# Optimization experiments

Hardware: AMD Instinct MI355X
Metric: run time of the kernel (lower is better)

The kernel has to match this reference:

```python
import jax, jax.numpy as jnp
import numpy as np
from jax import lax

B, Q, H, W = 2, 2304, 64, 64
ENC_OUT = 64          # encoder out_dim
DIM = 192             # base_dim
HEAD = 8
R = 3
RA = (2 * R + 1) ** 2  # 49 local-window positions
CF = 64                # pe enc_dims // 2 (complex channels)
ENC_DIMS = 2 * CF      # 128
IN_DIM = (DIM + ENC_DIMS) * RA + 2  # 15682
HID = 256


def conv3(x, w, b):
    y = lax.conv_general_dilated(x, w, (1, 1), 'SAME',
                                 dimension_numbers=('NCHW', 'OIHW', 'NCHW'))
    return y + b[None, :, None, None]


def _flat_gather(img, idx):
    # img [B,C,HW], idx [B,...] -> [B,C,...]
    return jax.vmap(lambda f, i: f[:, i])(img, idx)


def gather_nearest(img, c):
    # grid_sample nearest, align_corners=False, zeros padding. c [B,Q,K,2] (y,x)
    Bc, C, Hc, Wc = img.shape
    py = ((c[..., 0] + 1) * Hc - 1) / 2
    px = ((c[..., 1] + 1) * Wc - 1) / 2
    iy = jnp.round(py); ix = jnp.round(px)
    valid = (iy >= 0) & (iy < Hc) & (ix >= 0) & (ix < Wc)
    idx = (jnp.clip(iy, 0, Hc - 1) * Wc + jnp.clip(ix, 0, Wc - 1)).astype(jnp.int32)
    g = _flat_gather(img.reshape(Bc, C, Hc * Wc), idx)  # [B,C,Q,K]
    g = jnp.where(valid[:, None], g, 0.0)
    return g.transpose(0, 2, 3, 1)  # [B,Q,K,C]


def gather_bilinear_zeros(img, c):
    # grid_sample bilinear, align_corners=False, zeros padding. c [B,Q,K,2]
    Bc, C, Hc, Wc = img.shape
    py = ((c[..., 0] + 1) * Hc - 1) / 2
    px = ((c[..., 1] + 1) * Wc - 1) / 2
    y0f = jnp.floor(py); x0f = jnp.floor(px)
    wy = py - y0f; wx = px - x0f
    y0 = y0f.astype(jnp.int32); x0 = x0f.astype(jnp.int32)
    flat = img.reshape(Bc, C, Hc * Wc)
    def corner(yi, xi, w):
        valid = (yi >= 0) & (yi < Hc) & (xi >= 0) & (xi < Wc)
        idx = jnp.clip(yi, 0, Hc - 1) * Wc + jnp.clip(xi, 0, Wc - 1)
        return _flat_gather(flat, idx) * (w * valid)[:, None]
    out = (corner(y0, x0, (1 - wy) * (1 - wx)) + corner(y0, x0 + 1, (1 - wy) * wx)
           + corner(y0 + 1, x0, wy * (1 - wx)) + corner(y0 + 1, x0 + 1, wy * wx))
    return out.transpose(0, 2, 3, 1)


def gather_bilinear_border(img, c):
    # grid_sample bilinear, align_corners=False, border padding. c [B,Q,2]
    Bc, C, Hc, Wc = img.shape
    py = jnp.clip(((c[..., 0] + 1) * Hc - 1) / 2, 0, Hc - 1)
    px = jnp.clip(((c[..., 1] + 1) * Wc - 1) / 2, 0, Wc - 1)
    y0f = jnp.floor(py); x0f = jnp.floor(px)
    wy = py - y0f; wx = px - x0f
    y0 = y0f.astype(jnp.int32); x0 = x0f.astype(jnp.int32)
    y1 = jnp.minimum(y0 + 1, Hc - 1); x1 = jnp.minimum(x0 + 1, Wc - 1)
    flat = img.reshape(Bc, C, Hc * Wc)
    g = lambda yi, xi: _flat_gather(flat, yi * Wc + xi)  # [B,C,Q]
    out = (g(y0, x0) * ((1 - wy) * (1 - wx))[:, None]
           + g(y0, x1) * ((1 - wy) * wx)[:, None]
           + g(y1, x0) * (wy * (1 - wx))[:, None]
           + g(y1, x1) * (wy * wx)[:, None])
    return out.transpose(0, 2, 1)  # [B,Q,C]


def _forward(inp, coord, cell, enc_w, enc_b, qw, qb, kw, kb, vw, vb, fw, fb,
             pbw, pbb, pew, w1, b1, w2, b2):
    feat = conv3(inp, enc_w, enc_b)            # encoder (simplified)
    fq = conv3(feat, qw, qb); fk = conv3(feat, kw, kb)
    fv = conv3(feat, vw, vb); ff = conv3(feat, fw, fb)
    Bq, Qn = coord.shape[:2]
    Hf, Wf = feat.shape[-2:]
    dk = DIM // HEAD
    c = jnp.clip(coord, -1 + 1e-6, 1 - 1e-6)[:, :, None, :]   # [B,Q,1,2]
    # nearest feature-grid pixel-center coordinates (= grid_sample nearest of coord_lr)
    iy = jnp.round(((c[..., 0] + 1) * Hf - 1) / 2)
    ix = jnp.round(((c[..., 1] + 1) * Wf - 1) / 2)
    ck0 = jnp.stack([-1 + (2 * iy + 1) / Hf, -1 + (2 * ix + 1) / Wf], axis=-1)
    dh = jnp.linspace(-R, R, 2 * R + 1) * 2 / Hf
    dw = jnp.linspace(-R, R, 2 * R + 1) * 2 / Wf
    delta = jnp.stack(jnp.meshgrid(dh, dw, indexing='ij'), axis=-1).reshape(1, 1, RA, 2)
    ck = ck0 + delta                                          # [B,Q,49,2]
    q_ = gather_bilinear_zeros(fq, c)[:, :, 0].reshape(Bq, Qn, HEAD, dk)
    k_ = gather_nearest(fk, ck).reshape(Bq, Qn, RA, HEAD, dk)
    v_ = gather_nearest(fv, ck).reshape(Bq, Qn, RA, HEAD, dk)
    fr = gather_nearest(ff, ck)                               # [B,Q,49,CF]
    hw = jnp.array([Hf, Wf], dtype=coord.dtype)
    rel = (coord[:, :, None, :] - ck) * hw                    # [B,Q,49,2]
    rel_cell = cell * hw
    sim = jnp.einsum('bqhd,bqkhd->bqkh', q_, k_) / np.sqrt(dk).astype(np.float32)
    pb = rel @ pbw + pbb                                      # positional bias [B,Q,49,HEAD]
    attn = jax.nn.softmax(sim + pb, axis=2)                   # softmax over the 49 window slots
    attn_map = attn[0, 10, :, 0].reshape(2 * R + 1, 2 * R + 1, 1)
    v_weighted = (v_ * attn[..., None]).reshape(Bq, Qn, RA, DIM)
    frc = jnp.fft.fft2(fr.reshape(Bq, Qn, 2 * R + 1, 2 * R + 1, CF),
                       axes=(2, 3), norm='ortho').reshape(Bq, Qn, RA, CF)
    phase = rel @ pew                                         # Fourier PE: exp(i*phase)
    enc = lax.complex(jnp.cos(phase), jnp.sin(phase)) * frc
    enc = jnp.stack([enc.real, enc.imag], axis=-1).reshape(Bq, Qn, RA, ENC_DIMS)
    out = jnp.concatenate([v_weighted, enc], axis=-1).reshape(Bq, Qn, -1)
    out = jnp.concatenate([out, rel_cell], axis=-1)           # [B,Q,IN_DIM]
    pred = jax.nn.relu(out @ w1 + b1) @ w2 + b2               # imnet MLP
    ret = pred + gather_bilinear_border(inp, coord)           # global residual
    return ret, attn_map


def setup_inputs() -> dict:
    key = jax.random.key(0)
    ks = jax.random.split(key, 20)
    def n(k, shape, s=0.05):
        return jax.random.normal(k, shape, dtype=jnp.float32) * s
    inp = jax.random.normal(ks[0], (B, 3, H, W), dtype=jnp.float32)
    coord = jax.random.uniform(ks[1], (B, Q, 2), minval=-1.0, maxval=1.0, dtype=jnp.float32)
    cell = jnp.full((B, Q, 2), 2.0 / 128, dtype=jnp.float32)
    return {
        'inp': inp, 'coord': coord, 'cell': cell,
        'enc_w': n(ks[2], (ENC_OUT, 3, 3, 3)), 'enc_b': n(ks[3], (ENC_OUT,)),
        'qw': n(ks[4], (DIM, ENC_OUT, 3, 3)), 'qb': n(ks[5], (DIM,)),
        'kw': n(ks[6], (DIM, ENC_OUT, 3, 3)), 'kb': n(ks[7], (DIM,)),
        'vw': n(ks[8], (DIM, ENC_OUT, 3, 3)), 'vb': n(ks[9], (DIM,)),
        'fw': n(ks[10], (CF, ENC_OUT, 3, 3)), 'fb': n(ks[11], (CF,)),
        'pbw': n(ks[12], (2, HEAD), 0.5), 'pbb': n(ks[13], (HEAD,), 0.5),
        'pew': n(ks[14], (2, CF), 0.5),
        'w1': n(ks[15], (IN_DIM, HID), 0.01), 'b1': n(ks[16], (HID,)),
        'w2': n(ks[17], (HID, 3), 0.05), 'b2': n(ks[18], (3,)),
    }


def reference(inp, coord, cell, enc_w, enc_b, qw, qb, kw, kb, vw, vb, fw, fb,
              pbw, pbb, pew, w1, b1, w2, b2):
    return _forward(inp, coord, cell, enc_w, enc_b, qw, qb, kw, kb, vw, vb,
                    fw, fb, pbw, pbb, pew, w1, b1, w2, b2)
```

## Files before the change

kernel.cpp:

```cpp
#include <hip/hip_runtime.h>

typedef unsigned short u16t;
typedef unsigned int   u32t;
typedef __attribute__((ext_vector_type(8))) short short8;
typedef __attribute__((ext_vector_type(4))) float f32x4;

#define B_    2
#define QN    2304
#define NQ    4608
#define HWS   64
#define ENCC  64
#define DIMC  192
#define NHEAD 8
#define DKH   24
#define RAW   49
#define CFC   64
#define FRP   68
#define CMAP  640
#define KCONV 576
#define INDIM 15682
#define KPAD  15744
#define HIDN  256
#define PIX   8192
#define SPLITK 12
#define KSLICE (KPAD/SPLITK)

__device__ __forceinline__ float b2f(u16t u){ u32t v=((u32t)u)<<16; return __builtin_bit_cast(float,v); }
__device__ __forceinline__ u16t f2b(float f){ u32t v=__builtin_bit_cast(u32t,f); return (u16t)((v + 0x7FFFu + ((v>>16)&1u))>>16); }

#define GLOAD16(SRC, DST) __builtin_amdgcn_global_load_lds( \
  (const __attribute__((address_space(1))) unsigned int*)(const void*)(SRC), \
  (__attribute__((address_space(3))) unsigned int*)(void*)(DST), 16, 0, 0)

__global__ __launch_bounds__(256) void k_enc(const float* __restrict__ inp, const float* __restrict__ ew,
                      const float* __restrict__ eb, u16t* __restrict__ feat){
  int i = blockIdx.x*256+threadIdx.x;
  if(i>=B_*HWS*HWS*ENCC) return;
  int oc=i&63, x=(i>>6)&63, y=(i>>12)&63, b=i>>18;
  float acc = eb[oc];
  for(int c=0;c<3;c++)
    for(int dy=0;dy<3;dy++){
      int yy=y+dy-1; if(yy<0||yy>=HWS) continue;
      for(int dx=0;dx<3;dx++){
        int xx=x+dx-1; if(xx<0||xx>=HWS) continue;
        acc += inp[((b*3+c)*HWS+yy)*HWS+xx] * ew[((oc*3+c)*3+dy)*3+dx];
      }
    }
  feat[i]=f2b(acc);
}

__global__ __launch_bounds__(256) void k_w1t(const float* __restrict__ w1, u16t* __restrict__ w1t){
  __shared__ u16t t[64][65];
  int kb = blockIdx.x*64, nb = blockIdx.y*64;
  for(int i=threadIdx.x;i<4096;i+=256){
    int k=i>>6, n=i&63; int gk=kb+k;
    t[k][n] = (gk<INDIM) ? f2b(w1[(size_t)gk*HIDN + nb + n]) : (u16t)0;
  }
  __syncthreads();
  for(int i=threadIdx.x;i<4096;i+=256){
    int n=i>>6, k=i&63;
    w1t[(size_t)(nb+n)*KPAD + kb + k] = t[k][n];
  }
}

__global__ __launch_bounds__(256) void k_wconv(const float* qw,const float* kw,const float* vw,const float* fw,
                        const float* qb,const float* kb_,const float* vb,const float* fb,
                        u16t* __restrict__ wct, float* __restrict__ bias){
  int i = blockIdx.x*256+threadIdx.x;
  if(i < CMAP*KCONV){
    int oc=i/KCONV, kk=i%KCONV;
    int ic=kk&63, tap=kk>>6;
    const float* w; int ol=oc;
    if(oc<192) w=qw;
    else if(oc<384){w=kw; ol=oc-192;}
    else if(oc<576){w=vw; ol=oc-384;}
    else {w=fw; ol=oc-576;}
    wct[(size_t)oc*KCONV + kk] = f2b(w[(ol*64+ic)*9 + tap]);
  }
  if(i<CMAP){
    bias[i] = (i<192)? qb[i] : (i<384? kb_[i-192] : (i<576? vb[i-384] : fb[i-576]));
  }
}

__global__ __launch_bounds__(256) void k_im2col(const u16t* __restrict__ feat, u16t* __restrict__ A){
  int i = blockIdx.x*256+threadIdx.x;
  if(i>=PIX*72) return;
  int k8=i%72, pix=i/72;
  int tap=k8/8, ic8=(k8&7)<<3;
  int x=pix&63, y=(pix>>6)&63, b=pix>>12;
  int yy=y+tap/3-1, xx=x+tap%3-1;
  uint4 v;
  if(yy>=0&&yy<HWS&&xx>=0&&xx<HWS) v = *(const uint4*)&feat[(size_t)(((b*HWS+yy)*HWS+xx)*ENCC)+ic8];
  else v = make_uint4(0u,0u,0u,0u);
  *(uint4*)&A[(size_t)pix*KCONV + tap*64 + ic8] = v;
}

__global__ __launch_bounds__(256,2) void k_gemm128(const u16t* __restrict__ A, int lda,
    const u16t* __restrict__ BT, int ldb, const float* __restrict__ bias,
    void* __restrict__ Cout, int ldc, int kslice, int mode){
  __shared__ __align__(16) u16t As[128*32];
  __shared__ __align__(16) u16t Bs[128*32];
  int m0 = blockIdx.x*128, n0 = blockIdx.y*128;
  int tid = threadIdx.x;
  int wave = tid>>6, lane = tid&63;
  int wm = wave>>1, wn = wave&1;
  int kg = lane>>4, l16 = lane&15;
  int kbeg = blockIdx.z*kslice, kend = kbeg+kslice;
  f32x4 acc[4][4] = {};
  for(int k0=kbeg;k0<kend;k0+=32){
    __syncthreads();
    #pragma unroll
    for(int s=0;s<2;s++){
      int seg = (wave*2+s)*64 + lane;
      int row = seg>>2, qp = seg&3;
      int q = qp ^ ((row>>1)&3);
      GLOAD16(&A [(size_t)(m0+row)*lda + k0 + q*8], &As[(wave*2+s)*512]);
      GLOAD16(&BT[(size_t)(n0+row)*ldb + k0 + q*8], &Bs[(wave*2+s)*512]);
    }
    __syncthreads();
    short8 a[4], b[4];
    #pragma unroll
    for(int mf=0;mf<4;mf++){
      int row = wm*64+mf*16+l16;
      a[mf] = *(const short8*)&As[row*32 + (kg^((row>>1)&3))*8];
    }
    #pragma unroll
    for(int nf=0;nf<4;nf++){
      int row = wn*64+nf*16+l16;
      b[nf] = *(const short8*)&Bs[row*32 + (kg^((row>>1)&3))*8];
    }
    #pragma unroll
    for(int mf=0;mf<4;mf++)
      #pragma unroll
      for(int nf=0;nf<4;nf++)
        acc[mf][nf] = __builtin_amdgcn_mfma_f32_16x16x32_bf16(a[mf], b[nf], acc[mf][nf], 0,0,0);
  }
  int l4 = lane>>4;
  if(mode==0){
    u16t* C16 = (u16t*)Cout;
    #pragma unroll
    for(int mf=0;mf<4;mf++){
      #pragma unroll
      for(int nf=0;nf<4;nf++){
        #pragma unroll
        for(int r=0;r<4;r++){
          int gm = m0 + wm*64 + mf*16 + l4*4 + r;
          int gn = n0 + wn*64 + nf*16 + l16;
          C16[(size_t)gm*ldc+gn] = f2b(acc[mf][nf][r] + bias[gn]);
        }
      }
    }
  } else {
    float* C32 = (float*)Cout + (size_t)blockIdx.z * (size_t)(gridDim.x*128) * ldc;
    #pragma unroll
    for(int mf=0;mf<4;mf++){
      #pragma unroll
      for(int nf=0;nf<4;nf++){
        #pragma unroll
        for(int r=0;r<4;r++){
          int gm = m0 + wm*64 + mf*16 + l4*4 + r;
          int gn = n0 + wn*64 + nf*16 + l16;
          C32[(size_t)gm*ldc+gn] = acc[mf][nf][r];
        }
      }
    }
  }
}

__global__ __launch_bounds__(256) void k_redout(const float* __restrict__ hidp, const float* __restrict__ b1,
                      const float* __restrict__ w2, const float* __restrict__ b2v,
                      const float* __restrict__ inp, const float* __restrict__ coord,
                      float* __restrict__ outp, int M, int q0){
  int i = blockIdx.x*256+threadIdx.x;
  if(i>=M*64) return;
  int q=i>>6, lane=i&63, n4=lane*4;
  f32x4 acc = *(const f32x4*)&b1[n4];
  for(int s=0;s<SPLITK;s++)
    acc += *(const f32x4*)&hidp[((size_t)s*M + q)*HIDN + n4];
  float h0=fmaxf(acc.x,0.f), h1=fmaxf(acc.y,0.f), h2=fmaxf(acc.z,0.f), h3=fmaxf(acc.w,0.f);
  float p0 = h0*w2[n4*3+0] + h1*w2[(n4+1)*3+0] + h2*w2[(n4+2)*3+0] + h3*w2[(n4+3)*3+0];
  float p1 = h0*w2[n4*3+1] + h1*w2[(n4+1)*3+1] + h2*w2[(n4+2)*3+1] + h3*w2[(n4+3)*3+1];
  float p2 = h0*w2[n4*3+2] + h1*w2[(n4+1)*3+2] + h2*w2[(n4+2)*3+2] + h3*w2[(n4+3)*3+2];
  #pragma unroll
  for(int m=1;m<64;m<<=1){
    p0 += __shfl_xor(p0, m);
    p1 += __shfl_xor(p1, m);
    p2 += __shfl_xor(p2, m);
  }
  if(lane<3){
    int qg = q0 + q;
    int j = lane;
    float accj = (j==0? p0 : (j==1? p1 : p2)) + b2v[j];
    int b=qg/QN;
    float cy=coord[qg*2], cx=coord[qg*2+1];
    float py=fminf(fmaxf(((cy+1.f)*64.f-1.f)*0.5f,0.f),63.f);
    float px=fminf(fmaxf(((cx+1.f)*64.f-1.f)*0.5f,0.f),63.f);
    float y0f=floorf(py), x0f=floorf(px);
    float wy=py-y0f, wx=px-x0f;
    int y0=(int)y0f, x0=(int)x0f;
    int y1=min(y0+1,63), x1=min(x0+1,63);
    const float* ip=&inp[(size_t)(b*3+j)*4096];
    float g00=ip[y0*64+x0], g01=ip[y0*64+x1];
    float g10=ip[y1*64+x0], g11=ip[y1*64+x1];
    float res=g00*(1.f-wy)*(1.f-wx)+g01*(1.f-wy)*wx+g10*wy*(1.f-wx)+g11*wy*wx;
    outp[qg*3+j]=accj+res;
  }
}

__global__ __launch_bounds__(256) void k_feat(const float* __restrict__ coord, const float* __restrict__ cell,
                       const u16t* __restrict__ maps, const float* __restrict__ pbw,
                       const float* __restrict__ pbb, const float* __restrict__ pew,
                       u16t* __restrict__ F, float* __restrict__ outAttn, int q0){
  __shared__ float q_lds[DIMC];
  __shared__ float relsy[RAW], relsx[RAW];
  __shared__ int   wbase[RAW];
  __shared__ float sa[RAW][NHEAD];
  __shared__ float fr_lds[RAW*FRP];
  __shared__ float c7[7], s7[7];
  __shared__ float pewf0[CFC], pewf1[CFC];
  __shared__ float pbwf0[NHEAD], pbwf1[NHEAD], pbbf[NHEAD];

  int qg = q0 + blockIdx.x;
  int b  = qg / QN;
  int tid = threadIdx.x;
  float cy = coord[qg*2], cx = coord[qg*2+1];
  const float lo = -1.0f + 1e-6f, hi = 1.0f - 1e-6f;
  float ccy = fminf(fmaxf(cy,lo),hi), ccx = fminf(fmaxf(cx,lo),hi);
  float pyq = ((ccy+1.f)*64.f - 1.f)*0.5f, pxq = ((ccx+1.f)*64.f - 1.f)*0.5f;
  int iy = (int)rintf(pyq), ix = (int)rintf(pxq);

  if(tid < RAW){
    int ki = tid/7, kj = tid%7;
    int yy = iy + ki - 3, xx = ix + kj - 3;
    wbase[tid] = (yy>=0&&yy<64&&xx>=0&&xx<64) ? ((b*64+yy)*64+xx)*CMAP : -1;
    float ck_y = (-1.f + (float)(2*iy+1)*(1.f/64.f)) + (float)(ki-3)*(2.f/64.f);
    float ck_x = (-1.f + (float)(2*ix+1)*(1.f/64.f)) + (float)(kj-3)*(2.f/64.f);
    relsy[tid] = (cy - ck_y)*64.f;
    relsx[tid] = (cx - ck_x)*64.f;
  }
  if(tid<7){ float ang = -6.283185307179586f * (float)tid / 7.f; c7[tid]=cosf(ang); s7[tid]=sinf(ang); }
  if(tid<CFC){ pewf0[tid]=pew[tid]; pewf1[tid]=pew[CFC+tid]; }
  if(tid<NHEAD){ pbwf0[tid]=pbw[tid]; pbwf1[tid]=pbw[NHEAD+tid]; pbbf[tid]=pbb[tid]; }
  __syncthreads();

  if(tid < DIMC){
    float y0f=floorf(pyq), x0f=floorf(pxq);
    float wy=pyq-y0f, wx=pxq-x0f;
    int y0=(int)y0f, x0=(int)x0f;
    float acc=0.f;
    for(int ty=0;ty<2;ty++) for(int tx=0;tx<2;tx++){
      int yy=y0+ty, xx=x0+tx;
      if(yy<0||yy>=64||xx<0||xx>=64) continue;
      float w=(ty? wy:1.f-wy)*(tx? wx:1.f-wx);
      acc += w * b2f(maps[(size_t)((b*64+yy)*64+xx)*CMAP + tid]);
    }
    q_lds[tid]=acc;
  }
  for(int i=tid;i<RAW*8;i+=256){
    int k=i>>3, c8=(i&7)<<3;
    int base=wbase[k];
    f32x4 lo4={0.f,0.f,0.f,0.f}, hi4={0.f,0.f,0.f,0.f};
    if(base>=0){
      uint4 t = *(const uint4*)&maps[(size_t)base + 576 + c8];
      lo4 = f32x4{b2f((u16t)t.x), b2f((u16t)(t.x>>16)), b2f((u16t)t.y), b2f((u16t)(t.y>>16))};
      hi4 = f32x4{b2f((u16t)t.z), b2f((u16t)(t.z>>16)), b2f((u16t)t.w), b2f((u16t)(t.w>>16))};
    }
    *(f32x4*)&fr_lds[k*FRP+c8]   = lo4;
    *(f32x4*)&fr_lds[k*FRP+c8+4] = hi4;
  }
  __syncthreads();

  for(int i=tid;i<RAW*NHEAD;i+=256){
    int k=i>>3, h=i&7;
    int base=wbase[k];
    float dot=0.f;
    if(base>=0){
      const u16t* p = &maps[(size_t)base + DIMC + h*DKH];
      for(int c8=0;c8<3;c8++){
        uint4 t = *(const uint4*)&p[c8*8];
        u32t a4[4]={t.x,t.y,t.z,t.w};
        for(int j=0;j<4;j++){
          dot += q_lds[h*DKH + c8*8 + 2*j]   * b2f((u16t)a4[j]);
          dot += q_lds[h*DKH + c8*8 + 2*j+1] * b2f((u16t)(a4[j]>>16));
        }
      }
    }
    sa[k][h] = dot/sqrtf(24.f) + relsy[k]*pbwf0[h] + relsx[k]*pbwf1[h] + pbbf[h];
  }
  __syncthreads();

  if(tid < 64){
    int h = tid>>3, sub = tid&7;
    float m = -1e30f;
    for(int k=sub;k<RAW;k+=8) m = fmaxf(m, sa[k][h]);
    #pragma unroll
    for(int mm=1;mm<8;mm<<=1) m = fmaxf(m, __shfl_xor(m, mm));
    float s = 0.f;
    for(int k=sub;k<RAW;k+=8){ float e=__expf(sa[k][h]-m); sa[k][h]=e; s+=e; }
    #pragma unroll
    for(int mm=1;mm<8;mm<<=1) s += __shfl_xor(s, mm);
    float inv = 1.f/s;
    for(int k=sub;k<RAW;k+=8) sa[k][h]*=inv;
  }
  __syncthreads();
  if(qg==10 && tid<RAW) outAttn[tid] = sa[tid][0];

  size_t frow = (size_t)(qg-q0)*KPAD;
  for(int i=tid;i<RAW*24;i+=256){
    int k=i/24, c8=(i%24)*8;
    int base=wbase[k];
    u32t o[4]={0,0,0,0};
    if(base>=0){
      uint4 t = *(const uint4*)&maps[(size_t)base + 384 + c8];
      u32t a4[4]={t.x,t.y,t.z,t.w};
      for(int j=0;j<4;j++){
        int c0=c8+2*j;
        u16t r0=f2b(b2f((u16t)a4[j])      * sa[k][ c0   /DKH]);
        u16t r1=f2b(b2f((u16t)(a4[j]>>16))* sa[k][(c0+1)/DKH]);
        o[j] = (u32t)r0 | ((u32t)r1<<16);
      }
    }
    *(uint4*)&F[frow + (size_t)k*320 + c8] = make_uint4(o[0],o[1],o[2],o[3]);
  }
  if(tid<64){
    int idx=INDIM-2+tid;
    u16t v=0;
    if(idx==15680) v=f2b(cell[qg*2]*64.f);
    else if(idx==15681) v=f2b(cell[qg*2+1]*64.f);
    F[frow+idx]=v;
  }

  #pragma unroll
  for(int pp=0;pp<2;pp++){
    int p = tid + pp*256;
    if(p < 448){
      int v_ = p>>6, c = p&63;
      float Gr[7], Gi[7];
      #pragma unroll
      for(int a_=0;a_<7;a_++){
        float re=0.f, im=0.f;
        #pragma unroll
        for(int bb=0;bb<7;bb++){
          float f=fr_lds[(a_*7+bb)*FRP+c];
          int m=(v_*bb)%7;
          re += f*c7[m]; im += f*s7[m];
        }
        Gr[a_]=re; Gi[a_]=im;
      }
      float pw0=pewf0[c], pw1=pewf1[c];
      #pragma unroll
      for(int u=0;u<7;u++){
        int k = u*7 + v_;
        float tr=0.f, ti=0.f;
        #pragma unroll
        for(int a_=0;a_<7;a_++){
          int m=(u*a_)%7;
          float cc=c7[m], ss=s7[m];
          tr += Gr[a_]*cc - Gi[a_]*ss;
          ti += Gr[a_]*ss + Gi[a_]*cc;
        }
        tr*=(1.f/7.f); ti*=(1.f/7.f);
        float ph = relsy[k]*pw0 + relsx[k]*pw1;
        float sp, cp; __sincosf(ph, &sp, &cp);
        float er = cp*tr - sp*ti, ei = cp*ti + sp*tr;
        u32t pk = (u32t)f2b(er) | ((u32t)f2b(ei)<<16);
        *(u32t*)&F[frow + (size_t)k*320 + 192 + 2*c] = pk;
      }
    }
  }
}

__global__ __launch_bounds__(256) void k_mark(float* __restrict__ outp, int n, float val){
  int i = blockIdx.x*256+threadIdx.x;
  if(i<n) outp[i]=val;
}

extern "C" void kernel_launch(void* const* d_in, const int* in_sizes, int n_in,
                              void* d_out, int out_size, void* d_ws, size_t ws_size,
                              hipStream_t stream){
  int I_inp, I_coord, I_cell, I_encw, I_encb, I_qw, I_qb, I_kw, I_kb, I_vw, I_vb,
      I_fw, I_fb, I_pbw, I_pbb, I_pew, I_w1, I_b1, I_w2, I_b2;
  bool dictOrder = (n_in==20 && in_sizes[0]==24576 && in_sizes[1]==9216 && in_sizes[3]==1728
                    && in_sizes[5]==110592 && in_sizes[16]==4014592 && in_sizes[19]==3);
  bool sortOrder = (n_in==20 && in_sizes[0]==256 && in_sizes[1]==3 && in_sizes[8]==24576
                    && in_sizes[10]==110592 && in_sizes[18]==4014592 && in_sizes[19]==768);
  if(dictOrder){
    I_inp=0; I_coord=1; I_cell=2; I_encw=3; I_encb=4; I_qw=5; I_qb=6; I_kw=7; I_kb=8;
    I_vw=9; I_vb=10; I_fw=11; I_fb=12; I_pbw=13; I_pbb=14; I_pew=15; I_w1=16; I_b1=17; I_w2=18; I_b2=19;
  } else if(sortOrder){
    I_b1=0; I_b2=1; I_cell=2; I_coord=3; I_encb=4; I_encw=5; I_fb=6; I_fw=7; I_inp=8;
    I_kb=9; I_kw=10; I_pbb=11; I_pbw=12; I_pew=13; I_qb=14; I_qw=15; I_vb=16; I_vw=17; I_w1=18; I_w2=19;
  } else {
    float mark = (float)(n_in==20 ? in_sizes[0] : 1000000+n_in);
    k_mark<<<dim3((out_size+255)/256), dim3(256), 0, stream>>>((float*)d_out, out_size, mark);
    return;
  }

  const float* inp  =(const float*)d_in[I_inp];
  const float* coord=(const float*)d_in[I_coord];
  const float* cell =(const float*)d_in[I_cell];
  const float* enc_w=(const float*)d_in[I_encw];
  const float* enc_b=(const float*)d_in[I_encb];
  const float* qw=(const float*)d_in[I_qw];
  const float* qb=(const float*)d_in[I_qb];
  const float* kw=(const float*)d_in[I_kw];
  const float* kbp=(const float*)d_in[I_kb];
  const float* vw=(const float*)d_in[I_vw];
  const float* vb=(const float*)d_in[I_vb];
  const float* fw=(const float*)d_in[I_fw];
  const float* fb=(const float*)d_in[I_fb];
  const float* pbw=(const float*)d_in[I_pbw];
  const float* pbb=(const float*)d_in[I_pbb];
  const float* pew=(const float*)d_in[I_pew];
  const float* w1=(const float*)d_in[I_w1];
  const float* b1=(const float*)d_in[I_b1];
  const float* w2=(const float*)d_in[I_w2];
  const float* b2v=(const float*)d_in[I_b2];
  float* outp=(float*)d_out;

  char* ws=(char*)d_ws;
  size_t off=0;
  auto alloc=[&](size_t bytes){ size_t o=off; off=(off+bytes+255)&~(size_t)255; return o; };
  size_t o_feat = alloc((size_t)PIX*ENCC*2);
  size_t o_imc  = alloc((size_t)PIX*KCONV*2);
  size_t o_wct  = alloc((size_t)CMAP*KCONV*2);
  size_t o_cb   = alloc((size_t)CMAP*4);
  size_t o_maps = alloc((size_t)PIX*CMAP*2);
  size_t o_w1t  = alloc((size_t)HIDN*KPAD*2);
  size_t fixed = off;
  size_t rem = (ws_size>fixed)? ws_size-fixed : 0;
  size_t perQ = (size_t)KPAD*2 + (size_t)SPLITK*HIDN*4;
  long long cq = (long long)(rem/perQ);
  int chunkQ = (int)((cq/128)*128);
  if(chunkQ>NQ) chunkQ=NQ;
  size_t o_F, o_hp;
  if(chunkQ>=128){
    o_F  = alloc((size_t)chunkQ*KPAD*2);
    o_hp = alloc((size_t)SPLITK*chunkQ*HIDN*4);
  } else {
    chunkQ = 128;
    o_F  = o_imc;
    o_hp = (o_imc + (size_t)128*KPAD*2 + 255) & ~(size_t)255;
  }

  u16t*  feat=(u16t*)(ws+o_feat);
  u16t*  imc =(u16t*)(ws+o_imc);
  u16t*  wct =(u16t*)(ws+o_wct);
  float* cbias=(float*)(ws+o_cb);
  u16t*  maps=(u16t*)(ws+o_maps);
  u16t*  w1t =(u16t*)(ws+o_w1t);
  u16t*  Fb  =(u16t*)(ws+o_F);
  float* hidp=(float*)(ws+o_hp);

  k_w1t   <<<dim3(KPAD/64, HIDN/64), dim3(256), 0, stream>>>(w1, w1t);
  k_wconv <<<dim3((CMAP*KCONV+255)/256), dim3(256), 0, stream>>>(qw,kw,vw,fw,qb,kbp,vb,fb,wct,cbias);
  k_enc   <<<dim3((PIX*ENCC+255)/256), dim3(256), 0, stream>>>(inp,enc_w,enc_b,feat);
  k_im2col<<<dim3((PIX*72+255)/256), dim3(256), 0, stream>>>(feat,imc);
  k_gemm128<<<dim3(PIX/128, CMAP/128, 1), dim3(256), 0, stream>>>(imc, KCONV, wct, KCONV, cbias,
            (void*)maps, CMAP, KCONV, 0);

  for(int q0=0;q0<NQ;q0+=chunkQ){
    int nq = (NQ-q0 < chunkQ) ? (NQ-q0) : chunkQ;
    k_feat<<<dim3(nq), dim3(256), 0, stream>>>(coord,cell,maps,pbw,pbb,pew,Fb,outp+13824,q0);
    k_gemm128<<<dim3(nq/128, HIDN/128, SPLITK), dim3(256), 0, stream>>>(Fb, KPAD, w1t, KPAD, b1,
            (void*)hidp, HIDN, KSLICE, 2);
    k_redout<<<dim3((nq*64+255)/256), dim3(256), 0, stream>>>(hidp, b1, w2, b2v, inp, coord,
            outp, nq, q0);
  }
}
```

Before: 192.1 us.

## Deepen GEMM K-tile to 64, store split-K partials in bf16

The GEMM kernel now stages 64-wide K tiles in shared memory with an 8-way XOR swizzle and runs two MFMA sub-steps per barrier pair. This halves the number of synchronizations and gives more work per load. KPAD grows so that the padded K splits evenly into 64-wide slices across 12 split-K chunks, and the feature kernel zero-fills the larger padding. Split-K partial sums are written as bf16 instead of fp32, which halves partial-buffer traffic but loses accuracy in the reduction, and the larger padding adds some wasted FLOPs.

Result: faster. 179.1 us (-6.7%).

```diff
diff --git a/kernel.cpp b/kernel.cpp
--- a/kernel.cpp
+++ b/kernel.cpp
@@ -19,7 +19,7 @@
 #define CMAP  640
 #define KCONV 576
 #define INDIM 15682
-#define KPAD  15744
+#define KPAD  16128
 #define HIDN  256
 #define PIX   8192
 #define SPLITK 12
@@ -95,11 +95,11 @@
   *(uint4*)&A[(size_t)pix*KCONV + tap*64 + ic8] = v;
 }
 
-__global__ __launch_bounds__(256,2) void k_gemm128(const u16t* __restrict__ A, int lda,
+__global__ __launch_bounds__(256) void k_gemm128(const u16t* __restrict__ A, int lda,
     const u16t* __restrict__ BT, int ldb, const float* __restrict__ bias,
     void* __restrict__ Cout, int ldc, int kslice, int mode){
-  __shared__ __align__(16) u16t As[128*32];
-  __shared__ __align__(16) u16t Bs[128*32];
+  __shared__ __align__(16) u16t As[128*64];
+  __shared__ __align__(16) u16t Bs[128*64];
   int m0 = blockIdx.x*128, n0 = blockIdx.y*128;
   int tid = threadIdx.x;
   int wave = tid>>6, lane = tid&63;
@@ -107,33 +107,37 @@
   int kg = lane>>4, l16 = lane&15;
   int kbeg = blockIdx.z*kslice, kend = kbeg+kslice;
   f32x4 acc[4][4] = {};
-  for(int k0=kbeg;k0<kend;k0+=32){
+  for(int k0=kbeg;k0<kend;k0+=64){
     __syncthreads();
     #pragma unroll
-    for(int s=0;s<2;s++){
-      int seg = (wave*2+s)*64 + lane;
-      int row = seg>>2, qp = seg&3;
-      int q = qp ^ ((row>>1)&3);
-      GLOAD16(&A [(size_t)(m0+row)*lda + k0 + q*8], &As[(wave*2+s)*512]);
-      GLOAD16(&BT[(size_t)(n0+row)*ldb + k0 + q*8], &Bs[(wave*2+s)*512]);
+    for(int j=0;j<4;j++){
+      int seg = (wave*4+j)*64 + lane;
+      int row = seg>>3, qp = seg&7;
+      int q = qp ^ (row&7);
+      GLOAD16(&A [(size_t)(m0+row)*lda + k0 + q*8], &As[(wave*4+j)*512]);
+      GLOAD16(&BT[(size_t)(n0+row)*ldb + k0 + q*8], &Bs[(wave*4+j)*512]);
     }
     __syncthreads();
-    short8 a[4], b[4];
-    #pragma unroll
-    for(int mf=0;mf<4;mf++){
-      int row = wm*64+mf*16+l16;
-      a[mf] = *(const short8*)&As[row*32 + (kg^((row>>1)&3))*8];
-    }
-    #pragma unroll
-    for(int nf=0;nf<4;nf++){
-      int row = wn*64+nf*16+l16;
-      b[nf] = *(const short8*)&Bs[row*32 + (kg^((row>>1)&3))*8];
-    }
-    #pragma unroll
-    for(int mf=0;mf<4;mf++)
-      #pragma unroll
-      for(int nf=0;nf<4;nf++)
-        acc[mf][nf] = __builtin_amdgcn_mfma_f32_16x16x32_bf16(a[mf], b[nf], acc[mf][nf], 0,0,0);
+    #pragma unroll
+    for(int kk=0;kk<2;kk++){
+      int ks = kk*4 + kg;
+      short8 a[4], b[4];
+      #pragma unroll
+      for(int mf=0;mf<4;mf++){
+        int row = wm*64+mf*16+l16;
+        a[mf] = *(const short8*)&As[row*64 + (ks^(row&7))*8];
+      }
+      #pragma unroll
+      for(int nf=0;nf<4;nf++){
+        int row = wn*64+nf*16+l16;
+        b[nf] = *(const short8*)&Bs[row*64 + (ks^(row&7))*8];
+      }
+      #pragma unroll
+      for(int mf=0;mf<4;mf++)
+        #pragma unroll
+        for(int nf=0;nf<4;nf++)
+          acc[mf][nf] = __builtin_amdgcn_mfma_f32_16x16x32_bf16(a[mf], b[nf], acc[mf][nf], 0,0,0);
+    }
   }
   int l4 = lane>>4;
   if(mode==0){
@@ -151,7 +155,7 @@
       }
     }
   } else {
-    float* C32 = (float*)Cout + (size_t)blockIdx.z * (size_t)(gridDim.x*128) * ldc;
+    u16t* C16 = (u16t*)Cout + (size_t)blockIdx.z * (size_t)(gridDim.x*128) * ldc;
     #pragma unroll
     for(int mf=0;mf<4;mf++){
       #pragma unroll
@@ -160,14 +164,14 @@
         for(int r=0;r<4;r++){
           int gm = m0 + wm*64 + mf*16 + l4*4 + r;
           int gn = n0 + wn*64 + nf*16 + l16;
-          C32[(size_t)gm*ldc+gn] = acc[mf][nf][r];
+          C16[(size_t)gm*ldc+gn] = f2b(acc[mf][nf][r]);
         }
       }
     }
   }
 }
 
-__global__ __launch_bounds__(256) void k_redout(const float* __restrict__ hidp, const float* __restrict__ b1,
+__global__ __launch_bounds__(256) void k_redout(const u16t* __restrict__ hidp, const float* __restrict__ b1,
                       const float* __restrict__ w2, const float* __restrict__ b2v,
                       const float* __restrict__ inp, const float* __restrict__ coord,
                       float* __restrict__ outp, int M, int q0){
@@ -175,8 +179,11 @@
   if(i>=M*64) return;
   int q=i>>6, lane=i&63, n4=lane*4;
   f32x4 acc = *(const f32x4*)&b1[n4];
-  for(int s=0;s<SPLITK;s++)
-    acc += *(const f32x4*)&hidp[((size_t)s*M + q)*HIDN + n4];
+  for(int s=0;s<SPLITK;s++){
+    uint2 t = *(const uint2*)&hidp[((size_t)s*M + q)*HIDN + n4];
+    acc.x += b2f((u16t)t.x); acc.y += b2f((u16t)(t.x>>16));
+    acc.z += b2f((u16t)t.y); acc.w += b2f((u16t)(t.y>>16));
+  }
   float h0=fmaxf(acc.x,0.f), h1=fmaxf(acc.y,0.f), h2=fmaxf(acc.z,0.f), h3=fmaxf(acc.w,0.f);
   float p0 = h0*w2[n4*3+0] + h1*w2[(n4+1)*3+0] + h2*w2[(n4+2)*3+0] + h3*w2[(n4+3)*3+0];
   float p1 = h0*w2[n4*3+1] + h1*w2[(n4+1)*3+1] + h2*w2[(n4+2)*3+1] + h3*w2[(n4+3)*3+1];
@@ -322,8 +329,7 @@
     }
     *(uint4*)&F[frow + (size_t)k*320 + c8] = make_uint4(o[0],o[1],o[2],o[3]);
   }
-  if(tid<64){
-    int idx=INDIM-2+tid;
+  for(int idx=INDIM-2+tid; idx<KPAD; idx+=256){
     u16t v=0;
     if(idx==15680) v=f2b(cell[qg*2]*64.f);
     else if(idx==15681) v=f2b(cell[qg*2+1]*64.f);
@@ -429,14 +435,14 @@
   size_t o_w1t  = alloc((size_t)HIDN*KPAD*2);
   size_t fixed = off;
   size_t rem = (ws_size>fixed)? ws_size-fixed : 0;
-  size_t perQ = (size_t)KPAD*2 + (size_t)SPLITK*HIDN*4;
+  size_t perQ = (size_t)KPAD*2 + (size_t)SPLITK*HIDN*2;
   long long cq = (long long)(rem/perQ);
   int chunkQ = (int)((cq/128)*128);
   if(chunkQ>NQ) chunkQ=NQ;
   size_t o_F, o_hp;
   if(chunkQ>=128){
     o_F  = alloc((size_t)chunkQ*KPAD*2);
-    o_hp = alloc((size_t)SPLITK*chunkQ*HIDN*4);
+    o_hp = alloc((size_t)SPLITK*chunkQ*HIDN*2);
   } else {
     chunkQ = 128;
     o_F  = o_imc;
@@ -450,7 +456,7 @@
   u16t*  maps=(u16t*)(ws+o_maps);
   u16t*  w1t =(u16t*)(ws+o_w1t);
   u16t*  Fb  =(u16t*)(ws+o_F);
-  float* hidp=(float*)(ws+o_hp);
+  u16t*  hidp=(u16t*)(ws+o_hp);
 
   k_w1t   <<<dim3(KPAD/64, HIDN/64), dim3(256), 0, stream>>>(w1, w1t);
   k_wconv <<<dim3((CMAP*KCONV+255)/256), dim3(256), 0, stream>>>(qw,kw,vw,fw,qb,kbp,vb,fb,wct,cbias);
```
